# Optimization experiments

Hardware: AMD Instinct MI355X
Metric: run time of the kernel (lower is better)

The kernel has to match this reference:

```python
import jax, jax.numpy as jnp
import numpy as np
import math

B, C, IMG, P = 256, 3, 32, 4
D, H = 256, 8
HD = D // H
T = (IMG // P) ** 2          # 64 patches
T1 = T + 1                   # +cls token
MLP_H = 2048
HEAD_H = T * D // 2          # 8192
NUM_CLASSES = 10
PATCH_DIM = C * P * P


def _pe(t1, d):
    pos = jnp.arange(t1, dtype=jnp.float32)[:, None]
    div = jnp.exp(jnp.arange(0, d, 2, dtype=jnp.float32) * (-math.log(10000.0) / d))
    s = jnp.sin(pos * div)   # [T1, d/2]
    c = jnp.cos(pos * div)
    return jnp.stack([s, c], axis=-1).reshape(t1, d)  # interleave: even=sin, odd=cos


def _ln2d(x, w, b, eps=1e-5):
    # LayerNorm over last two dims [T1, D] with affine params of shape [T1, D]
    mu = jnp.mean(x, axis=(-2, -1), keepdims=True)
    var = jnp.mean((x - mu) ** 2, axis=(-2, -1), keepdims=True)
    return (x - mu) * jax.lax.rsqrt(var + eps) * w + b


def setup_inputs() -> dict:
    key = jax.random.key(0)
    ks = jax.random.split(key, 16)
    s = 0.02
    inp = {
        "x": jax.random.normal(ks[0], (B, C, IMG, IMG), dtype=jnp.float32),
        "cls_token": jax.random.normal(ks[1], (1, 1, D), dtype=jnp.float32),
        "Wp": jax.random.normal(ks[2], (PATCH_DIM, D), dtype=jnp.float32) * s,
        "bp": jnp.zeros((D,), jnp.float32),
        # 2 transformer blocks, params stacked on leading axis
        "qkv_w": jax.random.normal(ks[3], (2, D, 3 * D), dtype=jnp.float32) * s,
        "qkv_b": jnp.zeros((2, 3 * D), jnp.float32),
        "ln_w": jnp.ones((2, T1, D), jnp.float32),
        "ln_b": jnp.zeros((2, T1, D), jnp.float32),
        "mlp1_w": jax.random.normal(ks[4], (2, D, MLP_H), dtype=jnp.float32) * s,
        "mlp1_b": jnp.zeros((2, MLP_H), jnp.float32),
        "mlp2_w": jax.random.normal(ks[5], (2, MLP_H, D), dtype=jnp.float32) * s,
        "mlp2_b": jnp.zeros((2, D), jnp.float32),
        "head1_w": jax.random.normal(ks[6], (T1 * D, HEAD_H), dtype=jnp.float32) * s,
        "head1_b": jnp.zeros((HEAD_H,), jnp.float32),
        "head2_w": jax.random.normal(ks[7], (HEAD_H, NUM_CLASSES), dtype=jnp.float32) * s,
        "head2_b": jnp.zeros((NUM_CLASSES,), jnp.float32),
    }
    return inp


def reference(x, cls_token, Wp, bp, qkv_w, qkv_b, ln_w, ln_b,
              mlp1_w, mlp1_b, mlp2_w, mlp2_b, head1_w, head1_b, head2_w, head2_b):
    b = x.shape[0]
    n = IMG // P
    # patchify: [B,C,n,P,n,P] -> [B,n,n,C,P,P] -> [B, T, C*P*P]  (C-major per patch)
    patches = x.reshape(b, C, n, P, n, P).transpose(0, 2, 4, 1, 3, 5).reshape(b, T, PATCH_DIM)
    out = patches @ Wp + bp                                     # [B, T, D]
    cls = jnp.broadcast_to(cls_token, (b, 1, D))
    out = jnp.concatenate([cls, out], axis=1)                   # [B, T1, D]
    out = out + _pe(T1, D)[None]

    scale = 1.0 / math.sqrt(HD)
    for i in range(2):  # dropout is eval-mode identity
        h = _ln2d(out, ln_w[i], ln_b[i])
        qkv = (h @ qkv_w[i] + qkv_b[i]).reshape(b, T1, H, 3, HD)
        q, k, v = qkv[..., 0, :], qkv[..., 1, :], qkv[..., 2, :]   # [B,S,H,hd]
        scores = jnp.einsum('bqhd,bkhd->bhqk', q, k) * scale
        a = jax.nn.softmax(scores, axis=-1)
        attn = jnp.einsum('bhqk,bkhd->bqhd', a, v).reshape(b, T1, D)
        r = attn + out
        h2 = _ln2d(r, ln_w[i], ln_b[i])                          # same LN reused
        m = jax.nn.relu(h2 @ mlp1_w[i] + mlp1_b[i])
        out = (m @ mlp2_w[i] + mlp2_b[i]) + r

    flat = out.reshape(b, T1 * D)
    hidden = jax.nn.silu(flat @ head1_w + head1_b)
    return hidden @ head2_w + head2_b                            # [B, 10] logits
```

## Files before the change

kernel.cpp:

```cpp
#include <hip/hip_runtime.h>
#include <hip/hip_fp16.h>
#include <math.h>
#include <stdint.h>

#define B_ 256
#define C_ 3
#define IMG_ 32
#define D_ 256
#define H_ 8
#define HD_ 32
#define T1_ 65
#define MLP_H_ 2048
#define HEAD_H_ 8192
#define NCLS 10
#define PDIM 48
#define M_ROWS (B_*T1_)

typedef _Float16 f16;
typedef _Float16 f16x8 __attribute__((ext_vector_type(8)));
typedef _Float16 f16x4 __attribute__((ext_vector_type(4)));
typedef _Float16 f16x2 __attribute__((ext_vector_type(2)));
typedef float f32x4 __attribute__((ext_vector_type(4)));

typedef const void __attribute__((address_space(1))) glob_cv;
typedef void __attribute__((address_space(3))) lds_v;

__device__ __forceinline__ void async16(const void* g, void* l) {
    __builtin_amdgcn_global_load_lds((glob_cv*)g, (lds_v*)l, 16, 0, 0);
}

__global__ __launch_bounds__(256) void prep_weights(
        const float* __restrict__ qkv_w, const float* __restrict__ mlp1_w,
        const float* __restrict__ mlp2_w, const float* __restrict__ Wp,
        f16* __restrict__ w_qkv_t, f16* __restrict__ w_mlp1_t,
        f16* __restrict__ w_mlp2_t, f16* __restrict__ wpT) {
    int id = blockIdx.x;
    if (id >= 2432) {
        int idx = (id - 2432) * 256 + threadIdx.x;
        int d = idx >> 6, j = idx & 63;
        wpT[idx] = (j < PDIM) ? (f16)Wp[j * D_ + d] : (f16)0.f;
        return;
    }
    const float* W; f16* Wt; int K, N, nbx, rel;
    if (id < 384) {
        int L = id >= 192; rel = id - L * 192;
        W = qkv_w + (size_t)L * D_ * 768; Wt = w_qkv_t + (size_t)L * 768 * 256;
        K = 256; N = 768; nbx = 24;
    } else if (id < 1408) {
        int L = (id - 384) >= 512; rel = (id - 384) - L * 512;
        W = mlp1_w + (size_t)L * D_ * 2048; Wt = w_mlp1_t + (size_t)L * 2048 * 256;
        K = 256; N = 2048; nbx = 64;
    } else {
        int L = (id - 1408) >= 512; rel = (id - 1408) - L * 512;
        W = mlp2_w + (size_t)L * 2048 * 256; Wt = w_mlp2_t + (size_t)L * 256 * 2048;
        K = 2048; N = 256; nbx = 8;
    }
    int bx = rel % nbx, by = rel / nbx;
    int n0 = bx * 32, k0 = by * 32;
    __shared__ float L2d[32][33];
    int t = threadIdx.x;
    int r = t >> 3, c4 = (t & 7) * 4;
    const float4 v = *(const float4*)(W + (size_t)(k0 + r) * N + n0 + c4);
    L2d[r][c4] = v.x; L2d[r][c4 + 1] = v.y; L2d[r][c4 + 2] = v.z; L2d[r][c4 + 3] = v.w;
    __syncthreads();
    f16x4 h;
    h[0] = (f16)L2d[c4][r]; h[1] = (f16)L2d[c4 + 1][r];
    h[2] = (f16)L2d[c4 + 2][r]; h[3] = (f16)L2d[c4 + 3][r];
    *(f16x4*)(Wt + (size_t)(n0 + r) * K + k0 + c4) = h;
}

__global__ __launch_bounds__(256) void patch_mfma(
        const float* __restrict__ x, const float* __restrict__ cls,
        const f16* __restrict__ WpT, const float* __restrict__ bp,
        float* __restrict__ out) {
    int b = blockIdx.x;
    __shared__ float xs[3072];
    __shared__ __align__(16) f16 Ap[64 * 64];
    __shared__ __align__(16) f16 Bp[256 * 64];
    int tid = threadIdx.x;
    int lane = tid & 63, wid = tid >> 6;
    int lr = lane & 15, kq = lane >> 4;

    for (int i = tid; i < 768; i += 256)
        ((float4*)xs)[i] = ((const float4*)(x + (size_t)b * 3072))[i];
    for (int i = tid; i < 2048; i += 256)
        async16(WpT + (size_t)i * 8, &Bp[i * 8]);
    __syncthreads();
    for (int i = tid; i < 64 * 64; i += 256) {
        int t = i >> 6, j = i & 63;
        float val = 0.f;
        if (j < PDIM) {
            int py = t >> 3, px = t & 7;
            int c = j >> 4, rr = j & 15;
            int iy = rr >> 2, ix = rr & 3;
            val = xs[c * 1024 + (py * 4 + iy) * 32 + px * 4 + ix];
        }
        Ap[i] = (f16)val;
    }
    __syncthreads();

    for (int tile = wid; tile < 64; tile += 4) {
        int mi = tile >> 4, ni = tile & 15;
        f32x4 acc = {0.f, 0.f, 0.f, 0.f};
        #pragma unroll
        for (int ks = 0; ks < 2; ++ks) {
            f16x8 a = *(const f16x8*)&Ap[(mi * 16 + lr) * 64 + ks * 32 + kq * 8];
            f16x8 bb = *(const f16x8*)&Bp[(ni * 16 + lr) * 64 + ks * 32 + kq * 8];
            acc = __builtin_amdgcn_mfma_f32_16x16x32_f16(a, bb, acc, 0, 0, 0);
        }
        int d = ni * 16 + lr;
        float div = __expf((float)(d & ~1) * (-9.210340371976184f / 256.0f));
        #pragma unroll
        for (int r = 0; r < 4; ++r) {
            int t = 1 + mi * 16 + kq * 4 + r;
            float ang = (float)t * div;
            float pe = (d & 1) ? __cosf(ang) : __sinf(ang);
            out[((size_t)b * T1_ + t) * D_ + d] = acc[r] + bp[d] + pe;
        }
    }
    out[(size_t)b * T1_ * D_ + tid] = cls[tid] + ((tid & 1) ? 1.f : 0.f);
}

__global__ __launch_bounds__(1024) void ln_kernel(
        const float* __restrict__ xin, const float* __restrict__ w,
        const float* __restrict__ bb, f16* __restrict__ hout) {
    int b = blockIdx.x;
    const float4* x4 = (const float4*)(xin + (size_t)b * (T1_ * D_));
    const float4* w4 = (const float4*)w;
    const float4* b4 = (const float4*)bb;
    int tid = threadIdx.x;
    float s = 0.f, s2 = 0.f;
    for (int i = tid; i < 4160; i += 1024) {
        float4 v = x4[i];
        s  += v.x + v.y + v.z + v.w;
        s2 += v.x * v.x + v.y * v.y + v.z * v.z + v.w * v.w;
    }
    #pragma unroll
    for (int o = 32; o > 0; o >>= 1) { s += __shfl_down(s, o); s2 += __shfl_down(s2, o); }
    __shared__ float rs[16], rs2[16];
    __shared__ float mu_s, rstd_s;
    int wid = tid >> 6;
    if ((tid & 63) == 0) { rs[wid] = s; rs2[wid] = s2; }
    __syncthreads();
    if (tid == 0) {
        float S = 0.f, S2 = 0.f;
        #pragma unroll
        for (int i = 0; i < 16; ++i) { S += rs[i]; S2 += rs2[i]; }
        const float inv_n = 1.0f / (float)(T1_ * D_);
        float mu = S * inv_n;
        float var = S2 * inv_n - mu * mu;
        mu_s = mu; rstd_s = rsqrtf(var + 1e-5f);
    }
    __syncthreads();
    float mu = mu_s, rstd = rstd_s;
    f16* hb = hout + (size_t)b * (T1_ * D_);
    for (int i = tid; i < 4160; i += 1024) {
        float4 v = x4[i]; float4 wv = w4[i]; float4 bv = b4[i];
        f16x4 h;
        h[0] = (f16)((v.x - mu) * rstd * wv.x + bv.x);
        h[1] = (f16)((v.y - mu) * rstd * wv.y + bv.y);
        h[2] = (f16)((v.z - mu) * rstd * wv.z + bv.z);
        h[3] = (f16)((v.w - mu) * rstd * wv.w + bv.w);
        *(f16x4*)(hb + i * 4) = h;
    }
}

template<int EPI, typename OutT>
__global__ __launch_bounds__(256) void gemm_f16(
        const f16* __restrict__ A, const f16* __restrict__ Bt,
        const float* __restrict__ bias, const float* __restrict__ Res,
        OutT* __restrict__ Cc, f16* __restrict__ C2, int M, int N, int K) {
    __shared__ __align__(16) f16 As[2][128 * 32];
    __shared__ __align__(16) f16 Bs[2][128 * 32];
    int nb = blockIdx.x, mb = blockIdx.y;
    int t = threadIdx.x;
    int lane = t & 63, wid = t >> 6;
    int wr = wid >> 1, wc = wid & 1;
    int lr = lane & 15, kq = lane >> 4;
    int row0 = mb * 128, col0 = nb * 128;

    f32x4 acc[4][4];
    #pragma unroll
    for (int mi = 0; mi < 4; ++mi)
        #pragma unroll
        for (int ni = 0; ni < 4; ++ni)
            #pragma unroll
            for (int r = 0; r < 4; ++r) acc[mi][ni][r] = 0.f;

    int sr = t >> 2;
    int k8 = (t & 3) * 8;
    const f16* Ab = A + (size_t)row0 * K + k8;
    const f16* Bb = Bt + (size_t)col0 * K + k8;

    async16(Ab + (size_t)sr * K,        &As[0][t * 8]);
    async16(Ab + (size_t)(sr + 64) * K, &As[0][2048 + t * 8]);
    async16(Bb + (size_t)sr * K,        &Bs[0][t * 8]);
    async16(Bb + (size_t)(sr + 64) * K, &Bs[0][2048 + t * 8]);
    __syncthreads();

    int cur = 0;
    for (int k0 = 0; k0 < K; k0 += 32) {
        int nxt = cur ^ 1;
        if (k0 + 32 < K) {
            async16(Ab + (size_t)sr * K + k0 + 32,        &As[nxt][t * 8]);
            async16(Ab + (size_t)(sr + 64) * K + k0 + 32, &As[nxt][2048 + t * 8]);
            async16(Bb + (size_t)sr * K + k0 + 32,        &Bs[nxt][t * 8]);
            async16(Bb + (size_t)(sr + 64) * K + k0 + 32, &Bs[nxt][2048 + t * 8]);
        }
        f16x8 af[4], bf[4];
        #pragma unroll
        for (int mi = 0; mi < 4; ++mi)
            af[mi] = *(const f16x8*)&As[cur][(wr * 64 + mi * 16 + lr) * 32 + kq * 8];
        #pragma unroll
        for (int ni = 0; ni < 4; ++ni)
            bf[ni] = *(const f16x8*)&Bs[cur][(wc * 64 + ni * 16 + lr) * 32 + kq * 8];
        #pragma unroll
        for (int mi = 0; mi < 4; ++mi)
            #pragma unroll
            for (int ni = 0; ni < 4; ++ni)
                acc[mi][ni] = __builtin_amdgcn_mfma_f32_16x16x32_f16(af[mi], bf[ni], acc[mi][ni], 0, 0, 0);
        __syncthreads();
        cur = nxt;
    }

    #pragma unroll
    for (int mi = 0; mi < 4; ++mi) {
        #pragma unroll
        for (int ni = 0; ni < 4; ++ni) {
            int col = col0 + wc * 64 + ni * 16 + lr;
            #pragma unroll
            for (int r = 0; r < 4; ++r) {
                int row = row0 + wr * 64 + mi * 16 + kq * 4 + r;
                float v = acc[mi][ni][r] + bias[col];
                if (EPI == 1) v = fmaxf(v, 0.f);
                if (EPI == 2 || EPI == 3) v += Res[(size_t)row * N + col];
                Cc[(size_t)row * N + col] = (OutT)v;
                if (EPI == 3) C2[(size_t)row * N + col] = (f16)v;
            }
        }
    }
}

__device__ __forceinline__ int bswz(int col, int k) {
    return col * 32 + (k ^ (((col >> 2) & 3) << 3));
}

__global__ __launch_bounds__(256) void gemm_head1(
        const f16* __restrict__ A, const float* __restrict__ Bw,
        float* __restrict__ Cp) {
    __shared__ __align__(16) f16 As[2][256 * 32];
    __shared__ __align__(16) f16 Bs[2][64 * 32];
    const int K = M_ROWS, N = HEAD_H_;
    int nb = blockIdx.x;
    int z = blockIdx.y;
    int t = threadIdx.x;
    int lane = t & 63, wid = t >> 6;
    int lr = lane & 15, kq = lane >> 4;
    int col0 = nb * 64;
    int kstart = z * (K / 4);
    int kend = kstart + K / 4;

    f32x4 acc[4][4];
    #pragma unroll
    for (int mi = 0; mi < 4; ++mi)
        #pragma unroll
        for (int ni = 0; ni < 4; ++ni)
            #pragma unroll
            for (int r = 0; r < 4; ++r) acc[mi][ni][r] = 0.f;

    int sr = t >> 2;
    int k8 = (t & 3) * 8;
    const f16* Ab = A + k8;
    int kp = (t >> 4) * 2;
    int c0 = (t & 15) * 4;
    const float* Bb = Bw + col0 + c0;

    f32x4 bv0, bv1;

    auto stageA = [&](int buf, int k0) {
        #pragma unroll
        for (int r = 0; r < 4; ++r)
            async16(Ab + (size_t)(sr + r * 64) * K + k0, &As[buf][r * 2048 + t * 8]);
    };
    auto loadB = [&](int k0) {
        bv0 = *(const f32x4*)(Bb + (size_t)(k0 + kp) * N);
        bv1 = *(const f32x4*)(Bb + (size_t)(k0 + kp + 1) * N);
    };
    auto writeB = [&](int buf) {
        #pragma unroll
        for (int c = 0; c < 4; ++c) {
            f16x2 hv; hv[0] = (f16)bv0[c]; hv[1] = (f16)bv1[c];
            *(f16x2*)&Bs[buf][bswz(c0 + c, kp)] = hv;
        }
    };

    stageA(0, kstart);
    loadB(kstart);
    writeB(0);
    __syncthreads();

    int cur = 0;
    for (int k0 = kstart; k0 < kend; k0 += 32) {
        int nxt = cur ^ 1;
        bool pre = (k0 + 32 < kend);
        if (pre) {
            loadB(k0 + 32);
            stageA(nxt, k0 + 32);
        }
        f16x8 af[4], bf[4];
        #pragma unroll
        for (int mi = 0; mi < 4; ++mi)
            af[mi] = *(const f16x8*)&As[cur][(wid * 64 + mi * 16 + lr) * 32 + kq * 8];
        #pragma unroll
        for (int ni = 0; ni < 4; ++ni)
            bf[ni] = *(const f16x8*)&Bs[cur][bswz(ni * 16 + lr, kq * 8)];
        #pragma unroll
        for (int mi = 0; mi < 4; ++mi)
            #pragma unroll
            for (int ni = 0; ni < 4; ++ni)
                acc[mi][ni] = __builtin_amdgcn_mfma_f32_16x16x32_f16(af[mi], bf[ni], acc[mi][ni], 0, 0, 0);
        if (pre) writeB(nxt);
        __syncthreads();
        cur = nxt;
    }

    float* Cout = Cp + (size_t)z * 256 * N;
    #pragma unroll
    for (int mi = 0; mi < 4; ++mi) {
        #pragma unroll
        for (int ni = 0; ni < 4; ++ni) {
            int col = col0 + ni * 16 + lr;
            #pragma unroll
            for (int r = 0; r < 4; ++r) {
                int row = wid * 64 + mi * 16 + kq * 4 + r;
                Cout[(size_t)row * N + col] = acc[mi][ni][r];
            }
        }
    }
}

__global__ __launch_bounds__(256) void attn_kernel(
        const f16* __restrict__ qkv, const float* __restrict__ outres,
        float* __restrict__ r) {
    int b = blockIdx.x >> 3, h = blockIdx.x & 7;
    __shared__ __align__(16) f16 Qs[80 * 32];
    __shared__ __align__(16) f16 Ks[80 * 32];
    __shared__ __align__(16) f16 Vt[32 * 96];
    __shared__ float Sf[80 * 81];
    __shared__ __align__(16) f16 Pf[80 * 96];
    int tid = threadIdx.x;
    int lane = tid & 63, wid = tid >> 6;
    int lr = lane & 15, kq = lane >> 4;
    const float scale = 0.17677669529663687f;

    const f16* base = qkv + (size_t)b * T1_ * 768 + h * 96;
    for (int i = tid; i < T1_ * 12; i += 256) {
        int t = i / 12, c = i % 12;
        f16x8 vv = *(const f16x8*)(base + (size_t)t * 768 + c * 8);
        if (c < 4) {
            f16x8 q8;
            #pragma unroll
            for (int j = 0; j < 8; ++j) q8[j] = (f16)((float)vv[j] * scale);
            *(f16x8*)&Qs[t * 32 + c * 8] = q8;
        } else if (c < 8) {
            *(f16x8*)&Ks[t * 32 + (c - 4) * 8] = vv;
        } else {
            int d0 = (c - 8) * 8;
            #pragma unroll
            for (int j = 0; j < 8; ++j) Vt[(d0 + j) * 96 + t] = vv[j];
        }
    }
    for (int i = tid; i < 32 * 31; i += 256) {
        int d = i / 31, kt = 65 + i % 31;
        Vt[d * 96 + kt] = (f16)0.f;
    }
    __syncthreads();

    for (int tile = wid; tile < 25; tile += 4) {
        int mi = tile / 5, ni = tile % 5;
        f16x8 a = *(const f16x8*)&Qs[(mi * 16 + lr) * 32 + kq * 8];
        f16x8 bb = *(const f16x8*)&Ks[(ni * 16 + lr) * 32 + kq * 8];
        f32x4 c = {0.f, 0.f, 0.f, 0.f};
        c = __builtin_amdgcn_mfma_f32_16x16x32_f16(a, bb, c, 0, 0, 0);
        #pragma unroll
        for (int rr2 = 0; rr2 < 4; ++rr2)
            Sf[(mi * 16 + kq * 4 + rr2) * 81 + ni * 16 + lr] = c[rr2];
    }
    __syncthreads();

    for (int row = tid >> 2; row < T1_; row += 64) {
        int sub = tid & 3;
        float m = -1e30f;
        for (int kt = sub; kt < T1_; kt += 4) m = fmaxf(m, Sf[row * 81 + kt]);
        m = fmaxf(m, __shfl_xor(m, 1));
        m = fmaxf(m, __shfl_xor(m, 2));
        float sum = 0.f;
        for (int kt = sub; kt < T1_; kt += 4) {
            float e = __expf(Sf[row * 81 + kt] - m);
            Sf[row * 81 + kt] = e; sum += e;
        }
        sum += __shfl_xor(sum, 1);
        sum += __shfl_xor(sum, 2);
        float inv = 1.f / sum;
        for (int kt = sub; kt < T1_; kt += 4)
            Pf[row * 96 + kt] = (f16)(Sf[row * 81 + kt] * inv);
        for (int kt = T1_ + sub; kt < 96; kt += 4)
            Pf[row * 96 + kt] = (f16)0.f;
    }
    __syncthreads();

    for (int tile = wid; tile < 10; tile += 4) {
        int mi = tile >> 1, ni = tile & 1;
        f32x4 acc = {0.f, 0.f, 0.f, 0.f};
        #pragma unroll
        for (int ks = 0; ks < 3; ++ks) {
            f16x8 a = *(const f16x8*)&Pf[(mi * 16 + lr) * 96 + ks * 32 + kq * 8];
            f16x8 bv = *(const f16x8*)&Vt[(ni * 16 + lr) * 96 + ks * 32 + kq * 8];
            acc = __builtin_amdgcn_mfma_f32_16x16x32_f16(a, bv, acc, 0, 0, 0);
        }
        #pragma unroll
        for (int rr2 = 0; rr2 < 4; ++rr2) {
            int qt = mi * 16 + kq * 4 + rr2;
            if (qt < T1_) {
                size_t o = ((size_t)b * T1_ + qt) * D_ + h * HD_ + ni * 16 + lr;
                r[o] = acc[rr2] + outres[o];
            }
        }
    }
}

__global__ __launch_bounds__(256) void head2_fused(
        const float* __restrict__ part, const float* __restrict__ h1b,
        const float* __restrict__ w, const float* __restrict__ h2b,
        float* __restrict__ out) {
    int b = blockIdx.x;
    const int NP = 256 * HEAD_H_;
    int tid = threadIdx.x;
    float acc[NCLS];
    #pragma unroll
    for (int n = 0; n < NCLS; ++n) acc[n] = 0.f;
    for (int kk = tid; kk < HEAD_H_; kk += 256) {
        size_t o = (size_t)b * HEAD_H_ + kk;
        float v = part[o] + part[o + NP] + part[o + 2 * (size_t)NP] + part[o + 3 * (size_t)NP]
                + h1b[kk];
        v = v / (1.f + __expf(-v));
        const float* wr = w + (size_t)kk * NCLS;
        #pragma unroll
        for (int n = 0; n < NCLS; ++n) acc[n] += v * wr[n];
    }
    #pragma unroll
    for (int n = 0; n < NCLS; ++n)
        #pragma unroll
        for (int o = 32; o > 0; o >>= 1) acc[n] += __shfl_down(acc[n], o);
    __shared__ float red[4][NCLS];
    int wid = tid >> 6;
    if ((tid & 63) == 0)
        for (int n = 0; n < NCLS; ++n) red[wid][n] = acc[n];
    __syncthreads();
    if (tid < NCLS) {
        int n = tid;
        out[(size_t)b * NCLS + n] = red[0][n] + red[1][n] + red[2][n] + red[3][n] + h2b[n];
    }
}

extern "C" void kernel_launch(void* const* d_in, const int* in_sizes, int n_in,
                              void* d_out, int out_size, void* d_ws, size_t ws_size,
                              hipStream_t stream) {
    (void)in_sizes; (void)n_in; (void)out_size; (void)ws_size;
    const float* x       = (const float*)d_in[0];
    const float* cls     = (const float*)d_in[1];
    const float* Wp      = (const float*)d_in[2];
    const float* bp      = (const float*)d_in[3];
    const float* qkv_w   = (const float*)d_in[4];
    const float* qkv_b   = (const float*)d_in[5];
    const float* ln_w    = (const float*)d_in[6];
    const float* ln_b    = (const float*)d_in[7];
    const float* mlp1_w  = (const float*)d_in[8];
    const float* mlp1_b  = (const float*)d_in[9];
    const float* mlp2_w  = (const float*)d_in[10];
    const float* mlp2_b  = (const float*)d_in[11];
    const float* head1_w = (const float*)d_in[12];
    const float* head1_b = (const float*)d_in[13];
    const float* head2_w = (const float*)d_in[14];
    const float* head2_b = (const float*)d_in[15];
    float* outp = (float*)d_out;

    char* ws = (char*)d_ws;
    size_t off = 0;
    auto alloc = [&](size_t bytes) -> void* {
        void* p = ws + off; off += (bytes + 255) & ~(size_t)255; return p;
    };
    float* s_out = (float*)alloc((size_t)M_ROWS * D_ * 4);
    float* s_r   = (float*)alloc((size_t)M_ROWS * D_ * 4);
    f16*   s_h   = (f16*)  alloc((size_t)M_ROWS * D_ * 2);
    void*  s_big = alloc((size_t)M_ROWS * MLP_H_ * 2);
    f16*   w_qkv_t  = (f16*)alloc((size_t)2 * 768 * 256 * 2);
    f16*   w_mlp1_t = (f16*)alloc((size_t)2 * 2048 * 256 * 2);
    f16*   w_mlp2_t = (f16*)alloc((size_t)2 * 256 * 2048 * 2);
    f16*   wpT      = (f16*)alloc((size_t)256 * 64 * 2);
    f16*   s_flat   = s_h;
    f16*   s_qkv = (f16*)s_big;
    f16*   s_m   = (f16*)s_big;
    float* s_part = (float*)s_big;

    dim3 blk(256);

    prep_weights<<<dim3(2496), blk, 0, stream>>>(
        qkv_w, mlp1_w, mlp2_w, Wp, w_qkv_t, w_mlp1_t, w_mlp2_t, wpT);
    patch_mfma<<<dim3(B_), blk, 0, stream>>>(x, cls, wpT, bp, s_out);

    for (int i = 0; i < 2; ++i) {
        const float* lw = ln_w + (size_t)i * T1_ * D_;
        const float* lb = ln_b + (size_t)i * T1_ * D_;
        ln_kernel<<<dim3(B_), dim3(1024), 0, stream>>>(s_out, lw, lb, s_h);
        gemm_f16<0, f16><<<dim3(768 / 128, M_ROWS / 128), blk, 0, stream>>>(
            s_h, w_qkv_t + (size_t)i * 768 * 256, qkv_b + (size_t)i * 768,
            nullptr, s_qkv, nullptr, M_ROWS, 768, 256);
        attn_kernel<<<dim3(B_ * H_), blk, 0, stream>>>(s_qkv, s_out, s_r);
        ln_kernel<<<dim3(B_), dim3(1024), 0, stream>>>(s_r, lw, lb, s_h);
        gemm_f16<1, f16><<<dim3(MLP_H_ / 128, M_ROWS / 128), blk, 0, stream>>>(
            s_h, w_mlp1_t + (size_t)i * 2048 * 256, mlp1_b + (size_t)i * MLP_H_,
            nullptr, s_m, nullptr, M_ROWS, MLP_H_, 256);
        if (i == 0) {
            gemm_f16<2, float><<<dim3(D_ / 128, M_ROWS / 128), blk, 0, stream>>>(
                s_m, w_mlp2_t + (size_t)i * 256 * 2048, mlp2_b + (size_t)i * D_,
                s_r, s_out, nullptr, M_ROWS, D_, MLP_H_);
        } else {
            gemm_f16<3, float><<<dim3(D_ / 128, M_ROWS / 128), blk, 0, stream>>>(
                s_m, w_mlp2_t + (size_t)i * 256 * 2048, mlp2_b + (size_t)i * D_,
                s_r, s_out, s_flat, M_ROWS, D_, MLP_H_);
        }
    }

    gemm_head1<<<dim3(HEAD_H_ / 64, 4), blk, 0, stream>>>(s_flat, head1_w, s_part);
    head2_fused<<<dim3(B_), blk, 0, stream>>>(s_part, head1_b, head2_w, head2_b, outp);
}
```

Before: 1.117 ms.

## Add 64-wide-N GEMM for MLP2 and raise head1 split-K to eight

MLP2 now uses a new GEMM variant with 128x64 tiles, which doubles the number of blocks for the narrow N=256 output. The head1 split-K factor goes from 4 to 8, with a launch-bounds occupancy hint of 3, and head2 sums 8 partial buffers. The aim is to fill the GPU better on these under-parallelized GEMMs. The cost is more fp32 partial-sum traffic, and the s_part buffer must be large enough to hold 8 slices.

```diff
diff --git a/kernel.cpp b/kernel.cpp
--- a/kernel.cpp
+++ b/kernel.cpp
@@ -15,6 +15,7 @@
 #define NCLS 10
 #define PDIM 48
 #define M_ROWS (B_*T1_)
+#define HZ 8
 
 typedef _Float16 f16;
 typedef _Float16 f16x8 __attribute__((ext_vector_type(8)));
@@ -241,11 +242,84 @@
     }
 }
 
+template<int EPI, typename OutT>
+__global__ __launch_bounds__(256) void gemm_f16_n64(
+        const f16* __restrict__ A, const f16* __restrict__ Bt,
+        const float* __restrict__ bias, const float* __restrict__ Res,
+        OutT* __restrict__ Cc, f16* __restrict__ C2, int M, int N, int K) {
+    __shared__ __align__(16) f16 As[2][128 * 32];
+    __shared__ __align__(16) f16 Bs[2][64 * 32];
+    int nb = blockIdx.x, mb = blockIdx.y;
+    int t = threadIdx.x;
+    int lane = t & 63, wid = t >> 6;
+    int lr = lane & 15, kq = lane >> 4;
+    int row0 = mb * 128, col0 = nb * 64;
+
+    f32x4 acc[2][4];
+    #pragma unroll
+    for (int mi = 0; mi < 2; ++mi)
+        #pragma unroll
+        for (int ni = 0; ni < 4; ++ni)
+            #pragma unroll
+            for (int r = 0; r < 4; ++r) acc[mi][ni][r] = 0.f;
+
+    int sr = t >> 2;
+    int k8 = (t & 3) * 8;
+    const f16* Ab = A + (size_t)row0 * K + k8;
+    const f16* Bb = Bt + (size_t)col0 * K + k8;
+
+    async16(Ab + (size_t)sr * K,        &As[0][t * 8]);
+    async16(Ab + (size_t)(sr + 64) * K, &As[0][2048 + t * 8]);
+    async16(Bb + (size_t)sr * K,        &Bs[0][t * 8]);
+    __syncthreads();
+
+    int cur = 0;
+    for (int k0 = 0; k0 < K; k0 += 32) {
+        int nxt = cur ^ 1;
+        if (k0 + 32 < K) {
+            async16(Ab + (size_t)sr * K + k0 + 32,        &As[nxt][t * 8]);
+            async16(Ab + (size_t)(sr + 64) * K + k0 + 32, &As[nxt][2048 + t * 8]);
+            async16(Bb + (size_t)sr * K + k0 + 32,        &Bs[nxt][t * 8]);
+        }
+        f16x8 af[2], bf[4];
+        #pragma unroll
+        for (int mi = 0; mi < 2; ++mi)
+            af[mi] = *(const f16x8*)&As[cur][(wid * 32 + mi * 16 + lr) * 32 + kq * 8];
+        #pragma unroll
+        for (int ni = 0; ni < 4; ++ni)
+            bf[ni] = *(const f16x8*)&Bs[cur][(ni * 16 + lr) * 32 + kq * 8];
+        #pragma unroll
+        for (int mi = 0; mi < 2; ++mi)
+            #pragma unroll
+            for (int ni = 0; ni < 4; ++ni)
+                acc[mi][ni] = __builtin_amdgcn_mfma_f32_16x16x32_f16(af[mi], bf[ni], acc[mi][ni], 0, 0, 0);
+        __syncthreads();
+        cur = nxt;
+    }
+
+    #pragma unroll
+    for (int mi = 0; mi < 2; ++mi) {
+        #pragma unroll
+        for (int ni = 0; ni < 4; ++ni) {
+            int col = col0 + ni * 16 + lr;
+            #pragma unroll
+            for (int r = 0; r < 4; ++r) {
+                int row = row0 + wid * 32 + mi * 16 + kq * 4 + r;
+                float v = acc[mi][ni][r] + bias[col];
+                if (EPI == 1) v = fmaxf(v, 0.f);
+                if (EPI == 2 || EPI == 3) v += Res[(size_t)row * N + col];
+                Cc[(size_t)row * N + col] = (OutT)v;
+                if (EPI == 3) C2[(size_t)row * N + col] = (f16)v;
+            }
+        }
+    }
+}
+
 __device__ __forceinline__ int bswz(int col, int k) {
     return col * 32 + (k ^ (((col >> 2) & 3) << 3));
 }
 
-__global__ __launch_bounds__(256) void gemm_head1(
+__global__ __launch_bounds__(256, 3) void gemm_head1(
         const f16* __restrict__ A, const float* __restrict__ Bw,
         float* __restrict__ Cp) {
     __shared__ __align__(16) f16 As[2][256 * 32];
@@ -257,8 +331,8 @@
     int lane = t & 63, wid = t >> 6;
     int lr = lane & 15, kq = lane >> 4;
     int col0 = nb * 64;
-    int kstart = z * (K / 4);
-    int kend = kstart + K / 4;
+    int kstart = z * (K / HZ);
+    int kend = kstart + K / HZ;
 
     f32x4 acc[4][4];
     #pragma unroll
@@ -434,15 +508,16 @@
         const float* __restrict__ w, const float* __restrict__ h2b,
         float* __restrict__ out) {
     int b = blockIdx.x;
-    const int NP = 256 * HEAD_H_;
+    const size_t NP = (size_t)256 * HEAD_H_;
     int tid = threadIdx.x;
     float acc[NCLS];
     #pragma unroll
     for (int n = 0; n < NCLS; ++n) acc[n] = 0.f;
     for (int kk = tid; kk < HEAD_H_; kk += 256) {
         size_t o = (size_t)b * HEAD_H_ + kk;
-        float v = part[o] + part[o + NP] + part[o + 2 * (size_t)NP] + part[o + 3 * (size_t)NP]
-                + h1b[kk];
+        float v = h1b[kk];
+        #pragma unroll
+        for (int p = 0; p < HZ; ++p) v += part[o + (size_t)p * NP];
         v = v / (1.f + __expf(-v));
         const float* wr = w + (size_t)kk * NCLS;
         #pragma unroll
@@ -522,16 +597,16 @@
             s_h, w_mlp1_t + (size_t)i * 2048 * 256, mlp1_b + (size_t)i * MLP_H_,
             nullptr, s_m, nullptr, M_ROWS, MLP_H_, 256);
         if (i == 0) {
-            gemm_f16<2, float><<<dim3(D_ / 128, M_ROWS / 128), blk, 0, stream>>>(
+            gemm_f16_n64<2, float><<<dim3(D_ / 64, M_ROWS / 128), blk, 0, stream>>>(
                 s_m, w_mlp2_t + (size_t)i * 256 * 2048, mlp2_b + (size_t)i * D_,
                 s_r, s_out, nullptr, M_ROWS, D_, MLP_H_);
         } else {
-            gemm_f16<3, float><<<dim3(D_ / 128, M_ROWS / 128), blk, 0, stream>>>(
+            gemm_f16_n64<3, float><<<dim3(D_ / 64, M_ROWS / 128), blk, 0, stream>>>(
                 s_m, w_mlp2_t + (size_t)i * 256 * 2048, mlp2_b + (size_t)i * D_,
                 s_r, s_out, s_flat, M_ROWS, D_, MLP_H_);
         }
     }
 
-    gemm_head1<<<dim3(HEAD_H_ / 64, 4), blk, 0, stream>>>(s_flat, head1_w, s_part);
+    gemm_head1<<<dim3(HEAD_H_ / 64, HZ), blk, 0, stream>>>(s_flat, head1_w, s_part);
     head2_fused<<<dim3(B_), blk, 0, stream>>>(s_part, head1_b, head2_w, head2_b, outp);
 }
```

New measurement: 1.129 ms. Within noise of the previous version (+1.0%).
